# Kernel tuning notes

Hardware: AMD Instinct MI355X
Metric: run time of the kernel (lower is better)

The kernel has to match this reference:

```python
import jax, jax.numpy as jnp
import numpy as np

HEAD_SIZE = 64
EPS_GN = 1e-5 * 8 * 8  # GroupNorm eps = 1e-5 * head_size_divisor**2


def rwkv7_scan(w_raw, q, k, v, a, b):
    """RWKV-7 'wind backstepping' linear recurrence.
    Inputs [B,T,H,N]. Per step (matching the CUDA kernel):
      decay = exp(-exp(w_raw)); sa = S @ a; S = S*decay + sa b^T + v k^T; y = S @ q
    State S is [B,H,N_value,N_key]."""
    decay = jnp.exp(-jnp.exp(w_raw))
    B, T, H, N = q.shape
    xs = tuple(jnp.moveaxis(t, 1, 0) for t in (decay, q, k, v, a, b))  # [T,B,H,N]
    S0 = jnp.zeros((B, H, N, N), q.dtype)

    def step(S, inp):
        d, qt, kt, vt, at, bt = inp
        sa = jnp.einsum('bhij,bhj->bhi', S, at)
        S = S * d[:, :, None, :] + sa[..., None] * bt[:, :, None, :] + vt[..., None] * kt[:, :, None, :]
        y = jnp.einsum('bhij,bhj->bhi', S, qt)
        return S, y

    _, ys = jax.lax.scan(step, S0, xs)
    return jnp.moveaxis(ys, 0, 1)  # [B,T,H,N]


def setup_inputs() -> dict:
    key = jax.random.key(0)
    B, T, C, H, N = 4, 960, 2048, 32, 64
    Dw, Da, Dv, Dg = 96, 96, 64, 256
    ks = iter(jax.random.split(key, 40))

    def nrm(shape, s=0.02):
        return jax.random.normal(next(ks), shape, jnp.float32) * s

    def uni(shape):
        return jax.random.uniform(next(ks), shape, jnp.float32)

    return dict(
        x=nrm((B, T, C), 1.0),
        v_first=nrm((B, T, C), 1.0),
        x_r=uni((1, 1, C)), x_w=uni((1, 1, C)), x_k=uni((1, 1, C)),
        x_v=uni((1, 1, C)), x_a=uni((1, 1, C)), x_g=uni((1, 1, C)),
        w0=jnp.linspace(-7.0, -2.0, C, dtype=jnp.float32).reshape(1, 1, C) + 0.5,
        w1=nrm((C, Dw)), w2=nrm((Dw, C)),
        a0=nrm((1, 1, C)), a1=nrm((C, Da)), a2=nrm((Da, C)),
        v0=jnp.ones((1, 1, C), jnp.float32), v1=nrm((C, Dv)), v2=nrm((Dv, C)),
        g1=nrm((C, Dg)), g2=nrm((Dg, C)),
        k_k=jnp.full((1, 1, C), 0.85, jnp.float32),
        k_a=jnp.ones((1, 1, C), jnp.float32),
        r_k=nrm((H, N)),
        Wr=nrm((C, C)), Wk=nrm((C, C)), Wv=nrm((C, C)), Wo=nrm((C, C)),
        ln_w=jnp.ones((C,), jnp.float32), ln_b=jnp.zeros((C,), jnp.float32),
    )


def reference(x, v_first, x_r, x_w, x_k, x_v, x_a, x_g,
              w0, w1, w2, a0, a1, a2, v0, v1, v2, g1, g2,
              k_k, k_a, r_k, Wr, Wk, Wv, Wo, ln_w, ln_b):
    B, T, C = x.shape
    H = C // HEAD_SIZE
    # time_shift: ZeroPad2d((0,0,1,-1)) == shift right by 1 along T with zero at t=0
    x_prev = jnp.pad(x, ((0, 0), (1, 0), (0, 0)))[:, :T]
    xx = x_prev - x
    xr = x + xx * x_r; xw = x + xx * x_w; xk = x + xx * x_k
    xv = x + xx * x_v; xa = x + xx * x_a; xg = x + xx * x_g

    r = xr @ Wr.T
    w = -jax.nn.softplus(-(w0 + jnp.tanh(xw @ w1) @ w2)) - 0.5
    k = xk @ Wk.T
    v = xv @ Wv.T
    # layer_id != 0: residual-value mixing with first layer's value
    v = v + (v_first - v) * jax.nn.sigmoid(v0 + (xv @ v1) @ v2)
    a = jax.nn.sigmoid(a0 + (xa @ a1) @ a2)
    g = jax.nn.sigmoid(xg @ g1) @ g2

    kk = (k * k_k).reshape(B, T, H, HEAD_SIZE)
    kk = kk / jnp.maximum(jnp.linalg.norm(kk, axis=-1, keepdims=True), 1e-12)  # F.normalize
    kk = kk.reshape(B, T, C)
    k = k * (1 + (a - 1) * k_a)

    hs = lambda t: t.reshape(B, T, H, HEAD_SIZE)
    y = rwkv7_scan(hs(w), hs(r), hs(k), hs(v), hs(-kk), hs(kk * a)).reshape(B, T, C)

    # GroupNorm(H groups over C)
    yg = y.reshape(B, T, H, HEAD_SIZE)
    mu = yg.mean(-1, keepdims=True)
    var = yg.var(-1, keepdims=True)
    y = ((yg - mu) / jnp.sqrt(var + EPS_GN)).reshape(B, T, C) * ln_w + ln_b

    y = y + ((hs(r) * hs(k) * r_k).sum(-1, keepdims=True) * hs(v)).reshape(B, T, C)
    return (y * g) @ Wo.T
```

## Files before the change

kernel.cpp:

```cpp
#include <hip/hip_runtime.h>
#include <stdint.h>

#define BDIM 4
#define TDIM 960
#define CDIM 2048
#define HDIM 32
#define NDIM 64
#define BT   (BDIM*TDIM)

typedef unsigned short u16;
typedef __attribute__((ext_vector_type(8))) short short8;
typedef __attribute__((ext_vector_type(4))) float f32x4;
typedef __attribute__((ext_vector_type(2))) float f32x2;

__device__ __forceinline__ float b2f(u16 u){
  union{unsigned int i; float f;}x; x.i=((unsigned int)u)<<16; return x.f;
}
__device__ __forceinline__ u16 f2b(float f){
  union{float f; unsigned int i;}x; x.f=f;
  unsigned int r = x.i + 0x7fffu + ((x.i>>16)&1u);
  return (u16)(r>>16);
}
__device__ __forceinline__ unsigned pk2(float lo, float hi){
  return (unsigned)f2b(lo) | ((unsigned)f2b(hi)<<16);
}
__device__ __forceinline__ void unpack8(uint4 p, float* o){
  o[0]=b2f((u16)(p.x&0xffff)); o[1]=b2f((u16)(p.x>>16));
  o[2]=b2f((u16)(p.y&0xffff)); o[3]=b2f((u16)(p.y>>16));
  o[4]=b2f((u16)(p.z&0xffff)); o[5]=b2f((u16)(p.z>>16));
  o[6]=b2f((u16)(p.w&0xffff)); o[7]=b2f((u16)(p.w>>16));
}
__device__ __forceinline__ uint4 pack8(const float* o){
  uint4 p;
  p.x = pk2(o[0],o[1]);
  p.y = pk2(o[2],o[3]);
  p.z = pk2(o[4],o[5]);
  p.w = pk2(o[6],o[7]);
  return p;
}
__device__ __forceinline__ void ld8f(const float* p, float* o){
  float4 a = *(const float4*)p;
  float4 b = *(const float4*)(p+4);
  o[0]=a.x;o[1]=a.y;o[2]=a.z;o[3]=a.w;o[4]=b.x;o[5]=b.y;o[6]=b.z;o[7]=b.w;
}
__device__ __forceinline__ float sigm(float x){ return 1.f/(1.f+expf(-x)); }
__device__ __forceinline__ void stc(float* p, float v){ *p = v; }
__device__ __forceinline__ void stc(u16* p, float v){ *p = f2b(v); }
__device__ __forceinline__ f32x2 lo2(f32x4 v){ return __builtin_shufflevector(v, v, 0, 1); }
__device__ __forceinline__ f32x2 hi2(f32x4 v){ return __builtin_shufflevector(v, v, 2, 3); }
__device__ __forceinline__ f32x2 up2(unsigned w){
  return (f32x2){ __int_as_float((int)(w<<16)), __int_as_float((int)(w & 0xffff0000u)) };
}

__device__ __forceinline__ float row_red16(float x){
  x += __int_as_float(__builtin_amdgcn_update_dpp(0, __float_as_int(x), 0xB1,  0xF, 0xF, true));
  x += __int_as_float(__builtin_amdgcn_update_dpp(0, __float_as_int(x), 0x4E,  0xF, 0xF, true));
  x += __int_as_float(__builtin_amdgcn_update_dpp(0, __float_as_int(x), 0x141, 0xF, 0xF, true));
  x += __int_as_float(__builtin_amdgcn_update_dpp(0, __float_as_int(x), 0x140, 0xF, 0xF, true));
  return x;
}

struct CvtJobs { const float* s[3]; u16* d[3]; };
__global__ __launch_bounds__(256) void cvt_kernel(CvtJobs jobs){
  const float* src = jobs.s[blockIdx.z];
  u16* dst = jobs.d[blockIdx.z];
  size_t i = ((size_t)blockIdx.x*256 + threadIdx.x)*8;
  float v[8]; ld8f(src+i, v);
  *(uint4*)(dst+i) = pack8(v);
}

struct TJob { const float* src; u16* dst; int R, Cs, DR, DC; };
struct TJobs8 { TJob j[8]; };

__global__ __launch_bounds__(256) void transpose_pad_kernel(TJobs8 jobs){
  TJob jb = jobs.j[blockIdx.z];
  int idx = blockIdx.x*256 + threadIdx.x;
  int total = jb.DR*jb.DC;
  if (idx >= total) return;
  int i = idx / jb.DC, k = idx % jb.DC;
  float v = 0.f;
  if (i < jb.Cs && k < jb.R) v = jb.src[(size_t)k*jb.Cs + i];
  jb.dst[idx] = f2b(v);
}

__global__ __launch_bounds__(256) void mix_kernel(
  const float* x,
  const float* cr, const float* cw, const float* ck,
  const float* cv, const float* ca, const float* cg,
  u16* mr, u16* mw, u16* mk, u16* mv, u16* ma, u16* mg)
{
  size_t tid = (size_t)blockIdx.x*256 + threadIdx.x;
  size_t base = tid*8;
  int c = (int)(base % CDIM);
  int row = (int)(base / CDIM);
  int t = row % TDIM;
  float xc[8], xp[8], xx[8], cf[8], o[8];
  ld8f(x+base, xc);
  if (t > 0) {
    ld8f(x+base-CDIM, xp);
  } else {
    for(int j=0;j<8;j++) xp[j]=0.f;
  }
  #pragma unroll
  for(int j=0;j<8;j++) xx[j]=xp[j]-xc[j];
#define DOMIX(CP, OP) do { ld8f(CP+c, cf); \
  _Pragma("unroll") for(int j=0;j<8;j++) o[j]=xc[j]+xx[j]*cf[j]; \
  *(uint4*)(OP+base)=pack8(o); } while(0)
  DOMIX(cr, mr); DOMIX(cw, mw); DOMIX(ck, mk);
  DOMIX(cv, mv); DOMIX(ca, ma); DOMIX(cg, mg);
#undef DOMIX
}

struct GemmJob {
  const u16* A; const u16* Bt; void* C;
  int nbm, nbn, K, lda, ldb, ldc;
};
struct GemmJobs8 { GemmJob j[8]; };

template<typename TC>
__global__ __launch_bounds__(256, 2) void gemm_bt_kernel(GemmJobs8 jobs){
  GemmJob jb = jobs.j[blockIdx.z];
  int bm = blockIdx.x % jb.nbm;
  int bn = blockIdx.x / jb.nbm;
  if (bn >= jb.nbn) return;
  __shared__ __attribute__((aligned(16))) u16 As[128*64];
  __shared__ __attribute__((aligned(16))) u16 Bs[128*64];
  int tid = threadIdx.x;
  int wave = tid>>6, lane = tid&63;
  int wr = wave>>1, wc = wave&1;
  f32x4 acc[4][4];
  #pragma unroll
  for(int i=0;i<4;i++)
    #pragma unroll
    for(int j=0;j<4;j++) acc[i][j] = (f32x4){0.f,0.f,0.f,0.f};
  const int rA0 = bm*128;
  const int rB0 = bn*128;
  int srow = (lane>>3);
  int scol = (lane&7)*8;
  for (int k0=0; k0<jb.K; k0+=64){
    #pragma unroll
    for (int it=0; it<4; ++it){
      int rr = wave*32 + it*8;
      const u16* gA = jb.A + (size_t)(rA0 + rr + srow)*jb.lda + (k0 + scol);
      __builtin_amdgcn_global_load_lds((const __attribute__((address_space(1))) void*)gA,
          (__attribute__((address_space(3))) void*)&As[rr*64], 16, 0, 0);
      const u16* gB = jb.Bt + (size_t)(rB0 + rr + srow)*jb.ldb + (k0 + scol);
      __builtin_amdgcn_global_load_lds((const __attribute__((address_space(1))) void*)gB,
          (__attribute__((address_space(3))) void*)&Bs[rr*64], 16, 0, 0);
    }
    __syncthreads();
    #pragma unroll
    for (int kc=0; kc<2; ++kc){
      short8 af[4], bfr[4];
      int ko = kc*32 + (lane>>4)*8;
      #pragma unroll
      for (int mi=0; mi<4; ++mi)
        af[mi] = *(const short8*)&As[(wr*64 + mi*16 + (lane&15))*64 + ko];
      #pragma unroll
      for (int ni=0; ni<4; ++ni)
        bfr[ni] = *(const short8*)&Bs[(wc*64 + ni*16 + (lane&15))*64 + ko];
      #pragma unroll
      for (int mi=0; mi<4; ++mi)
        #pragma unroll
        for (int ni=0; ni<4; ++ni)
          acc[mi][ni] = __builtin_amdgcn_mfma_f32_16x16x32_bf16(af[mi], bfr[ni], acc[mi][ni], 0, 0, 0);
    }
    __syncthreads();
  }
  TC* C = (TC*)jb.C;
  int cn = (lane&15);
  int rq = (lane>>4)*4;
  #pragma unroll
  for (int mi=0; mi<4; ++mi){
    #pragma unroll
    for (int ni=0; ni<4; ++ni){
      int col = rB0 + wc*64 + ni*16 + cn;
      int row = rA0 + wr*64 + mi*16 + rq;
      #pragma unroll
      for (int e=0; e<4; ++e)
        stc(&C[(size_t)(row+e)*jb.ldc + col], acc[mi][ni][e]);
    }
  }
}

__global__ __launch_bounds__(256) void act_kernel(u16* hw, u16* hg){
  int idx = blockIdx.x*256 + threadIdx.x;
  if (blockIdx.z==0){ if (idx < BT*128) hw[idx] = f2b(tanhf(b2f(hw[idx]))); }
  else              { if (idx < BT*256) hg[idx] = f2b(sigm(b2f(hg[idx]))); }
}

__global__ __launch_bounds__(256) void post_kernel(
  const u16* rbuf, const u16* kbuf, const u16* vraw, const float* vfirst,
  const u16* wl, const u16* al, const u16* vl,
  const float* w0, const float* a0, const float* v0,
  const float* kkc, const float* kac,
  float* dout, uint4* qki, uint4* abi, u16* vs)
{
  int row = blockIdx.x, tid = threadIdx.x;
  int c = tid*8;
  size_t base = (size_t)row*CDIM + c;
  float qf[8], kf[8], vr[8], vf[8], wlf[8], alf[8], vlf[8], w0f[8], a0f[8], v0f[8], kkf[8], kaf[8];
  unpack8(*(const uint4*)(rbuf+base), qf);
  unpack8(*(const uint4*)(kbuf+base), kf);
  unpack8(*(const uint4*)(vraw+base), vr);
  ld8f(vfirst+base, vf);
  unpack8(*(const uint4*)(wl+base), wlf);
  unpack8(*(const uint4*)(al+base), alf);
  unpack8(*(const uint4*)(vl+base), vlf);
  ld8f(w0+c, w0f);
  ld8f(a0+c, a0f);
  ld8f(v0+c, v0f);
  ld8f(kkc+c, kkf);
  ld8f(kac+c, kaf);
  float dv[8], av[8], vv[8], kkr[8], kfin[8], asv[8], bsv[8];
  float ssq = 0.f;
  #pragma unroll
  for (int j=0;j<8;j++){
    float wv = -log1pf(expf(-(w0f[j]+wlf[j]))) - 0.5f;
    dv[j]  = expf(-expf(wv));
    av[j]  = sigm(a0f[j]+alf[j]);
    vv[j]  = vr[j] + (vf[j]-vr[j])*sigm(v0f[j]+vlf[j]);
    kkr[j] = kf[j]*kkf[j];
    ssq   += kkr[j]*kkr[j];
    kfin[j]= kf[j]*(1.f + (av[j]-1.f)*kaf[j]);
  }
  ssq += __shfl_xor(ssq,1); ssq += __shfl_xor(ssq,2); ssq += __shfl_xor(ssq,4);
  float inv = 1.f/fmaxf(sqrtf(ssq), 1e-12f);
  #pragma unroll
  for (int j=0;j<8;j++){ float kkn = kkr[j]*inv; asv[j] = -kkn; bsv[j] = kkn*av[j]; }
  *(float4*)(dout+base)   = make_float4(dv[0],dv[1],dv[2],dv[3]);
  *(float4*)(dout+base+4) = make_float4(dv[4],dv[5],dv[6],dv[7]);
  uint4* qke = (uint4*)((char*)qki + (size_t)row*8192 + (size_t)c*4);
  qke[0] = make_uint4(pk2(qf[0],qf[1]), pk2(kfin[0],kfin[1]), pk2(qf[2],qf[3]), pk2(kfin[2],kfin[3]));
  qke[1] = make_uint4(pk2(qf[4],qf[5]), pk2(kfin[4],kfin[5]), pk2(qf[6],qf[7]), pk2(kfin[6],kfin[7]));
  uint4* abe = (uint4*)((char*)abi + (size_t)row*8192 + (size_t)c*4);
  abe[0] = make_uint4(pk2(asv[0],asv[1]), pk2(bsv[0],bsv[1]), pk2(asv[2],asv[3]), pk2(bsv[2],bsv[3]));
  abe[1] = make_uint4(pk2(asv[4],asv[5]), pk2(bsv[4],bsv[5]), pk2(asv[6],asv[7]), pk2(bsv[6],bsv[7]));
  *(uint4*)(vs+base) = pack8(vv);
}

__global__ __launch_bounds__(256, 2) void scan_kernel(
  const float* __restrict__ decayp, const uint4* __restrict__ qki,
  const uint4* __restrict__ abi, const u16* __restrict__ vs,
  float* __restrict__ yb)
{
  int blk = blockIdx.x;
  int b    = blk >> 7;
  int h    = (blk >> 2) & 31;
  int qtr  = blk & 3;
  int tid  = threadIdx.x;
  int jg   = tid & 15;
  int ii   = tid >> 4;
  int row  = qtr*16 + ii;

  const char* dP = (const char*)decayp + (size_t)b*TDIM*8192 + h*256 + jg*16;
  const char* qP = (const char*)qki    + (size_t)b*TDIM*8192 + h*256 + jg*16;
  const char* aP = (const char*)abi    + (size_t)b*TDIM*8192 + h*256 + jg*16;
  const char* vP = (const char*)vs     + (size_t)b*TDIM*4096 + h*128 + row*2;

  f32x2 Sa = (f32x2){0.f,0.f}, Sb = (f32x2){0.f,0.f};

  struct SR { f32x4 d; uint4 qk; uint4 ab; u16 v; };
  auto ld = [&](int t)->SR{
    SR r; size_t o = (size_t)t*8192;
    r.d  = *(const f32x4*)(dP + o);
    r.qk = *(const uint4*)(qP + o);
    r.ab = *(const uint4*)(aP + o);
    r.v  = *(const u16*)(vP + (size_t)t*4096);
    return r;
  };
  auto dostep = [&](const SR& r)->float{
    f32x2 a01 = up2(r.ab.x), a23 = up2(r.ab.z);
    f32x2 t = Sa*a01 + Sb*a23;
    float sap = t[0] + t[1];
    sap = row_red16(sap);
    f32x2 b01 = up2(r.ab.y), b23 = up2(r.ab.w);
    f32x2 k01 = up2(r.qk.y), k23 = up2(r.qk.w);
    float vi = b2f(r.v);
    f32x2 s2 = (f32x2){sap, sap};
    f32x2 v2 = (f32x2){vi, vi};
    Sa = Sa*lo2(r.d) + s2*b01 + v2*k01;
    Sb = Sb*hi2(r.d) + s2*b23 + v2*k23;
    f32x2 q01 = up2(r.qk.x), q23 = up2(r.qk.z);
    f32x2 u = Sa*q01 + Sb*q23;
    return u[0] + u[1];
  };

  SR A0=ld(0), A1=ld(1), A2=ld(2), A3=ld(3), A4=ld(4), A5=ld(5), A6=ld(6), A7=ld(7);
  for (int g=0; g<120; ++g){
    int tn = g*8 + 8;
    float yp[8];
#define STEPR(AR, S_) { yp[S_] = dostep(AR); int t_ = tn + (S_); \
    AR = ld(t_ < TDIM ? t_ : TDIM-1); }
    STEPR(A0,0) STEPR(A1,1) __builtin_amdgcn_sched_barrier(0);
    STEPR(A2,2) STEPR(A3,3) __builtin_amdgcn_sched_barrier(0);
    STEPR(A4,4) STEPR(A5,5) __builtin_amdgcn_sched_barrier(0);
    STEPR(A6,6) STEPR(A7,7) __builtin_amdgcn_sched_barrier(0);
#undef STEPR
    #pragma unroll
    for (int s=0; s<8; ++s) yp[s] = row_red16(yp[s]);
    if (jg < 8){
      float out = 0.f;
      #pragma unroll
      for (int s=0; s<8; ++s) if (jg==s) out = yp[s];
      yb[(size_t)b*TDIM*CDIM + (size_t)(g*8+jg)*CDIM + h*NDIM + row] = out;
    }
  }
}

__global__ __launch_bounds__(256) void final_kernel(
  const float* yb, const uint4* qki, const u16* vs,
  const float* rk, const float* lnw, const float* lnb, const u16* gl, u16* yg)
{
  int row = blockIdx.x, tid = threadIdx.x;
  int c = tid*8;
  size_t base = (size_t)row*CDIM + c;
  float y[8], rf[8], kf[8], vf[8], rkf[8], lw[8], lb[8], gf[8];
  ld8f(yb+base, y);
  const uint4* qke = (const uint4*)((const char*)qki + (size_t)row*8192 + (size_t)c*4);
  uint4 e0 = qke[0], e1 = qke[1];
  rf[0]=b2f((u16)(e0.x&0xffff)); rf[1]=b2f((u16)(e0.x>>16));
  rf[2]=b2f((u16)(e0.z&0xffff)); rf[3]=b2f((u16)(e0.z>>16));
  rf[4]=b2f((u16)(e1.x&0xffff)); rf[5]=b2f((u16)(e1.x>>16));
  rf[6]=b2f((u16)(e1.z&0xffff)); rf[7]=b2f((u16)(e1.z>>16));
  kf[0]=b2f((u16)(e0.y&0xffff)); kf[1]=b2f((u16)(e0.y>>16));
  kf[2]=b2f((u16)(e0.w&0xffff)); kf[3]=b2f((u16)(e0.w>>16));
  kf[4]=b2f((u16)(e1.y&0xffff)); kf[5]=b2f((u16)(e1.y>>16));
  kf[6]=b2f((u16)(e1.w&0xffff)); kf[7]=b2f((u16)(e1.w>>16));
  unpack8(*(const uint4*)(vs+base), vf);
  ld8f(rk+c,  rkf);
  ld8f(lnw+c, lw);
  ld8f(lnb+c, lb);
  unpack8(*(const uint4*)(gl+base), gf);
  float sy=0.f, syy=0.f, coef=0.f;
  #pragma unroll
  for (int j=0;j<8;j++){ sy+=y[j]; syy+=y[j]*y[j]; coef += rf[j]*kf[j]*rkf[j]; }
  sy  += __shfl_xor(sy,1);  sy  += __shfl_xor(sy,2);  sy  += __shfl_xor(sy,4);
  syy += __shfl_xor(syy,1); syy += __shfl_xor(syy,2); syy += __shfl_xor(syy,4);
  coef+= __shfl_xor(coef,1);coef+= __shfl_xor(coef,2);coef+= __shfl_xor(coef,4);
  float mu  = sy*(1.f/64.f);
  float var = syy*(1.f/64.f) - mu*mu;
  float rs  = rsqrtf(var + 6.4e-4f);
  float o[8];
  #pragma unroll
  for (int j=0;j<8;j++)
    o[j] = (((y[j]-mu)*rs)*lw[j] + lb[j] + coef*vf[j]) * gf[j];
  *(uint4*)(yg+base) = pack8(o);
}

extern "C" void kernel_launch(void* const* d_in, const int* in_sizes, int n_in,
                              void* d_out, int out_size, void* d_ws, size_t ws_size,
                              hipStream_t stream)
{
  const float* x      = (const float*)d_in[0];
  const float* vfirst = (const float*)d_in[1];
  const float* c_r = (const float*)d_in[2];
  const float* c_w = (const float*)d_in[3];
  const float* c_k = (const float*)d_in[4];
  const float* c_v = (const float*)d_in[5];
  const float* c_a = (const float*)d_in[6];
  const float* c_g = (const float*)d_in[7];
  const float* w0i = (const float*)d_in[8];
  const float* w1i = (const float*)d_in[9];
  const float* w2i = (const float*)d_in[10];
  const float* a0i = (const float*)d_in[11];
  const float* a1i = (const float*)d_in[12];
  const float* a2i = (const float*)d_in[13];
  const float* v0i = (const float*)d_in[14];
  const float* v1i = (const float*)d_in[15];
  const float* v2i = (const float*)d_in[16];
  const float* g1i = (const float*)d_in[17];
  const float* g2i = (const float*)d_in[18];
  const float* kki = (const float*)d_in[19];
  const float* kai = (const float*)d_in[20];
  const float* rki = (const float*)d_in[21];
  const float* Wr  = (const float*)d_in[22];
  const float* Wk  = (const float*)d_in[23];
  const float* Wv  = (const float*)d_in[24];
  const float* Wo  = (const float*)d_in[25];
  const float* lnw = (const float*)d_in[26];
  const float* lnb = (const float*)d_in[27];

  char* ws = (char*)d_ws;
  const size_t S2 = (size_t)BT*CDIM*2;
  u16* MIXR = (u16*)(ws + 0*S2);
  u16* MIXW = (u16*)(ws + 1*S2);
  u16* MIXK = (u16*)(ws + 2*S2);
  u16* MIXV = (u16*)(ws + 3*S2);
  u16* MIXA = (u16*)(ws + 4*S2);
  u16* MIXG = (u16*)(ws + 5*S2);
  u16* RBUF = (u16*)(ws + 6*S2);
  u16* KBUF = (u16*)(ws + 7*S2);
  u16* VRAW = (u16*)(ws + 8*S2);
  char* WB = ws + 9*S2;
  u16* WSLOT = (u16*)WB;
  char* WT = WB + 8388608;
  u16* W1T = (u16*)(WT + 0);
  u16* A1T = (u16*)(WT + 524288);
  u16* V1T = (u16*)(WT + 1048576);
  u16* G1T = (u16*)(WT + 1572864);
  u16* W2T = (u16*)(WT + 2621440);
  u16* A2T = (u16*)(WT + 3145728);
  u16* V2T = (u16*)(WT + 3670016);
  u16* G2T = (u16*)(WT + 4194304);
  char* HB = WT + 5242880;
  u16* HW = (u16*)(HB + 0);
  u16* HA = (u16*)(HB + 983040);
  u16* HV = (u16*)(HB + 1966080);
  u16* HG = (u16*)(HB + 2949120);
  char* L2 = HB + 4915200;
  u16* WL = (u16*)(L2 + 0*S2);
  u16* AL = (u16*)(L2 + 1*S2);
  u16* VL = (u16*)(L2 + 2*S2);
  u16* GL = (u16*)(L2 + 3*S2);
  u16* WK2 = (u16*)(L2 + 0);
  u16* WV2 = (u16*)(L2 + 8388608);
  float* WDEC = (float*)(ws + 0*S2);
  uint4* QKI  = (uint4*)(ws + 2*S2);
  uint4* ABI  = (uint4*)(ws + 4*S2);
  u16*   VS6  = (u16*)(ws + 6*S2);
  float* YBUF = (float*)(L2 + 0*S2);
  u16* YG = (u16*)(L2 + 2*S2);
  (void)in_sizes; (void)n_in; (void)out_size; (void)ws_size;

  TJobs8 tj;
  tj.j[0] = (TJob){w1i, W1T, 2048,  96, 128, 2048};
  tj.j[1] = (TJob){a1i, A1T, 2048,  96, 128, 2048};
  tj.j[2] = (TJob){v1i, V1T, 2048,  64, 128, 2048};
  tj.j[3] = (TJob){g1i, G1T, 2048, 256, 256, 2048};
  tj.j[4] = (TJob){w2i, W2T,   96, 2048, 2048, 128};
  tj.j[5] = (TJob){a2i, A2T,   96, 2048, 2048, 128};
  tj.j[6] = (TJob){v2i, V2T,   64, 2048, 2048, 128};
  tj.j[7] = (TJob){g2i, G2T,  256, 2048, 2048, 256};
  transpose_pad_kernel<<<dim3(2048,1,8), 256, 0, stream>>>(tj);

  mix_kernel<<<dim3(BT*CDIM/8/256), 256, 0, stream>>>(
      x, c_r, c_w, c_k, c_v, c_a, c_g, MIXR, MIXW, MIXK, MIXV, MIXA, MIXG);

  CvtJobs cj;
  cj.s[0] = Wr; cj.d[0] = WSLOT;
  cj.s[1] = Wk; cj.d[1] = WK2;
  cj.s[2] = Wv; cj.d[2] = WV2;
  cvt_kernel<<<dim3(2048,1,3), 256, 0, stream>>>(cj);

  GemmJobs8 mj;
  mj.j[0] = (GemmJob){MIXR, WSLOT, RBUF, 30, 16, 2048, 2048, 2048, 2048};
  mj.j[1] = (GemmJob){MIXK, WK2,   KBUF, 30, 16, 2048, 2048, 2048, 2048};
  mj.j[2] = (GemmJob){MIXV, WV2,   VRAW, 30, 16, 2048, 2048, 2048, 2048};
  mj.j[3] = (GemmJob){MIXW, W1T, HW, 30, 1, 2048, 2048, 2048, 128};
  mj.j[4] = (GemmJob){MIXA, A1T, HA, 30, 1, 2048, 2048, 2048, 128};
  mj.j[5] = (GemmJob){MIXV, V1T, HV, 30, 1, 2048, 2048, 2048, 128};
  mj.j[6] = (GemmJob){MIXG, G1T, HG, 30, 2, 2048, 2048, 2048, 256};
  mj.j[7] = mj.j[0];
  gemm_bt_kernel<u16><<<dim3(480,1,7), 256, 0, stream>>>(mj);

  act_kernel<<<dim3(3840,1,2), 256, 0, stream>>>(HW, HG);

  GemmJobs8 lj2;
  lj2.j[0] = (GemmJob){HW, W2T, WL, 30, 16, 128, 128, 128, 2048};
  lj2.j[1] = (GemmJob){HA, A2T, AL, 30, 16, 128, 128, 128, 2048};
  lj2.j[2] = (GemmJob){HV, V2T, VL, 30, 16, 128, 128, 128, 2048};
  lj2.j[3] = (GemmJob){HG, G2T, GL, 30, 16, 256, 256, 256, 2048};
  lj2.j[4] = lj2.j[0]; lj2.j[5] = lj2.j[0]; lj2.j[6] = lj2.j[0]; lj2.j[7] = lj2.j[0];
  gemm_bt_kernel<u16><<<dim3(480,1,4), 256, 0, stream>>>(lj2);

  post_kernel<<<dim3(BT), 256, 0, stream>>>(
      RBUF, KBUF, VRAW, vfirst, WL, AL, VL, w0i, a0i, v0i, kki, kai,
      WDEC, QKI, ABI, VS6);

  scan_kernel<<<dim3(512), 256, 0, stream>>>(
      WDEC, QKI, ABI, VS6, YBUF);

  final_kernel<<<dim3(BT), 256, 0, stream>>>(
      YBUF, QKI, VS6, rki, lnw, lnb, GL, YG);

  CvtJobs co;
  co.s[0] = Wo; co.d[0] = WSLOT;
  co.s[1] = Wo; co.d[1] = WSLOT;
  co.s[2] = Wo; co.d[2] = WSLOT;
  cvt_kernel<<<dim3(2048,1,1), 256, 0, stream>>>(co);
  GemmJobs8 oj;
  oj.j[0] = (GemmJob){YG, WSLOT, d_out, 30, 16, 2048, 2048, 2048, 2048};
  for (int i=1;i<8;i++) oj.j[i] = oj.j[0];
  gemm_bt_kernel<float><<<dim3(480,1,1), 256, 0, stream>>>(oj);
}
```

Baseline: 726.9 us.

## Split scan state rows across 32 lanes instead of 16 per row

The scan kernel now uses 512 threads per block, with 32 lanes per state row each holding two key columns instead of 16 lanes holding four. This halves per-thread serial work and loads per step, shortening the recurrence's critical path. In exchange, every step's reduction needs an extra cross-half swizzle (ds_swizzle xor 16), which adds LDS-path latency on the serial dependency chain. The occupancy request also doubles the number of threads per CU.

```diff
diff --git a/kernel.cpp b/kernel.cpp
--- a/kernel.cpp
+++ b/kernel.cpp
@@ -58,6 +58,9 @@
   x += __int_as_float(__builtin_amdgcn_update_dpp(0, __float_as_int(x), 0x141, 0xF, 0xF, true));
   x += __int_as_float(__builtin_amdgcn_update_dpp(0, __float_as_int(x), 0x140, 0xF, 0xF, true));
   return x;
+}
+__device__ __forceinline__ float xor16(float x){
+  return __int_as_float(__builtin_amdgcn_ds_swizzle(__float_as_int(x), 0x401F));
 }
 
 struct CvtJobs { const float* s[3]; u16* d[3]; };
@@ -239,9 +242,9 @@
   *(uint4*)(vs+base) = pack8(vv);
 }
 
-__global__ __launch_bounds__(256, 2) void scan_kernel(
-  const float* __restrict__ decayp, const uint4* __restrict__ qki,
-  const uint4* __restrict__ abi, const u16* __restrict__ vs,
+__global__ __launch_bounds__(512, 2) void scan_kernel(
+  const float* __restrict__ decayp, const uint2* __restrict__ qki,
+  const uint2* __restrict__ abi, const u16* __restrict__ vs,
   float* __restrict__ yb)
 {
   int blk = blockIdx.x;
@@ -249,40 +252,38 @@
   int h    = (blk >> 2) & 31;
   int qtr  = blk & 3;
   int tid  = threadIdx.x;
-  int jg   = tid & 15;
-  int ii   = tid >> 4;
+  int jg   = tid & 31;
+  int ii   = tid >> 5;
   int row  = qtr*16 + ii;
 
-  const char* dP = (const char*)decayp + (size_t)b*TDIM*8192 + h*256 + jg*16;
-  const char* qP = (const char*)qki    + (size_t)b*TDIM*8192 + h*256 + jg*16;
-  const char* aP = (const char*)abi    + (size_t)b*TDIM*8192 + h*256 + jg*16;
+  const char* dP = (const char*)decayp + (size_t)b*TDIM*8192 + h*256 + jg*8;
+  const char* qP = (const char*)qki    + (size_t)b*TDIM*8192 + h*256 + jg*8;
+  const char* aP = (const char*)abi    + (size_t)b*TDIM*8192 + h*256 + jg*8;
   const char* vP = (const char*)vs     + (size_t)b*TDIM*4096 + h*128 + row*2;
 
-  f32x2 Sa = (f32x2){0.f,0.f}, Sb = (f32x2){0.f,0.f};
-
-  struct SR { f32x4 d; uint4 qk; uint4 ab; u16 v; };
+  f32x2 S = (f32x2){0.f, 0.f};
+
+  struct SR { float2 d; uint2 qk; uint2 ab; u16 v; };
   auto ld = [&](int t)->SR{
     SR r; size_t o = (size_t)t*8192;
-    r.d  = *(const f32x4*)(dP + o);
-    r.qk = *(const uint4*)(qP + o);
-    r.ab = *(const uint4*)(aP + o);
+    r.d  = *(const float2*)(dP + o);
+    r.qk = *(const uint2*)(qP + o);
+    r.ab = *(const uint2*)(aP + o);
     r.v  = *(const u16*)(vP + (size_t)t*4096);
     return r;
   };
   auto dostep = [&](const SR& r)->float{
-    f32x2 a01 = up2(r.ab.x), a23 = up2(r.ab.z);
-    f32x2 t = Sa*a01 + Sb*a23;
+    f32x2 a01 = up2(r.ab.x);
+    f32x2 t = S * a01;
     float sap = t[0] + t[1];
     sap = row_red16(sap);
-    f32x2 b01 = up2(r.ab.y), b23 = up2(r.ab.w);
-    f32x2 k01 = up2(r.qk.y), k23 = up2(r.qk.w);
+    sap += xor16(sap);
+    f32x2 b01 = up2(r.ab.y);
+    f32x2 k01 = up2(r.qk.y);
     float vi = b2f(r.v);
-    f32x2 s2 = (f32x2){sap, sap};
-    f32x2 v2 = (f32x2){vi, vi};
-    Sa = Sa*lo2(r.d) + s2*b01 + v2*k01;
-    Sb = Sb*hi2(r.d) + s2*b23 + v2*k23;
-    f32x2 q01 = up2(r.qk.x), q23 = up2(r.qk.z);
-    f32x2 u = Sa*q01 + Sb*q23;
+    S = S*(f32x2){r.d.x, r.d.y} + (f32x2){sap,sap}*b01 + (f32x2){vi,vi}*k01;
+    f32x2 q01 = up2(r.qk.x);
+    f32x2 u = S * q01;
     return u[0] + u[1];
   };
 
@@ -298,7 +299,10 @@
     STEPR(A6,6) STEPR(A7,7) __builtin_amdgcn_sched_barrier(0);
 #undef STEPR
     #pragma unroll
-    for (int s=0; s<8; ++s) yp[s] = row_red16(yp[s]);
+    for (int s=0; s<8; ++s){
+      yp[s] = row_red16(yp[s]);
+      yp[s] += xor16(yp[s]);
+    }
     if (jg < 8){
       float out = 0.f;
       #pragma unroll
@@ -468,8 +472,8 @@
       RBUF, KBUF, VRAW, vfirst, WL, AL, VL, w0i, a0i, v0i, kki, kai,
       WDEC, QKI, ABI, VS6);
 
-  scan_kernel<<<dim3(512), 256, 0, stream>>>(
-      WDEC, QKI, ABI, VS6, YBUF);
+  scan_kernel<<<dim3(512), 512, 0, stream>>>(
+      WDEC, (const uint2*)QKI, (const uint2*)ABI, VS6, YBUF);
 
   final_kernel<<<dim3(BT), 256, 0, stream>>>(
       YBUF, QKI, VS6, rki, lnw, lnb, GL, YG);
```

Result: slower. 912.7 us (+25.6%).
